# Optimization experiments

Measured on AMD Instinct MI355X. Metric: run time of the kernel, lower is better.

## Reference

```python
import jax, jax.numpy as jnp
import numpy as np

B, S, H, NH = 2, 4096, 768, 12
DH = H // NH  # 64


def setup_inputs() -> dict:
    key = jax.random.key(0)
    ks = jax.random.split(key, 7)
    scale = 0.02
    return {
        "x": jax.random.normal(ks[0], (B, S, H), dtype=jnp.float32),
        "Wq": jax.random.normal(ks[1], (H, H), dtype=jnp.float32) * scale,
        "bq": jax.random.normal(ks[2], (H,), dtype=jnp.float32) * scale,
        "Wk": jax.random.normal(ks[3], (H, H), dtype=jnp.float32) * scale,
        "bk": jax.random.normal(ks[4], (H,), dtype=jnp.float32) * scale,
        "Wv": jax.random.normal(ks[5], (H, H), dtype=jnp.float32) * scale,
        "bv": jax.random.normal(ks[6], (H,), dtype=jnp.float32) * scale,
    }


def _split_heads(t):
    # [B,S,H] -> [B,NH,S,DH]
    return t.reshape(B, S, NH, DH).transpose(0, 2, 1, 3)


def reference(x, Wq, bq, Wk, bk, Wv, bv):
    q = _split_heads(x @ Wq + bq)
    k = _split_heads(x @ Wk + bk)
    v = _split_heads(x @ Wv + bv)
    # raw scores + zero additive mask (mask is all zeros, so it is a no-op)
    scores = jnp.einsum("bhqd,bhkd->bhqk", q, k) / jnp.sqrt(jnp.float32(DH))
    probs = jax.nn.softmax(scores, axis=-1)
    ctx = jnp.einsum("bhqk,bhkd->bhqd", probs, v)
    out = ctx.transpose(0, 2, 1, 3).reshape(B, S, H)
    return jnp.tanh(out)
```

## Files before the change

kernel.cpp:

```cpp
#include <hip/hip_runtime.h>
#include <hip/hip_bf16.h>

#define B_ 2
#define S_ 4096
#define H_ 768
#define NH_ 12
#define DH_ 64
#define M_ (B_ * S_)
#define N3_ (3 * H_)
#define NQK 1536
#define K_ H_
#define LOG2E 1.4426950408889634f

typedef __attribute__((ext_vector_type(8))) short short8;
typedef __attribute__((ext_vector_type(4))) float f32x4;
typedef __attribute__((ext_vector_type(16))) float f32x16;
typedef __attribute__((ext_vector_type(4))) unsigned int uint4v;
typedef __attribute__((ext_vector_type(4))) unsigned short ushort4v;

typedef __attribute__((address_space(3))) unsigned int lds_u32;
typedef const __attribute__((address_space(1))) unsigned int glb_u32;

__device__ __forceinline__ unsigned short f2bf(float f) {
    unsigned int u = __builtin_bit_cast(unsigned int, f);
    u += 0x7FFFu + ((u >> 16) & 1u);
    return (unsigned short)(u >> 16);
}
__device__ __forceinline__ unsigned int cvtpk_bf16(float lo, float hi) {
    unsigned int r;
    asm("v_cvt_pk_bf16_f32 %0, %1, %2" : "=v"(r) : "v"(lo), "v"(hi));
    return r;
}
__device__ __forceinline__ void plswap32(unsigned int &x, unsigned int &y) {
    asm("v_permlane32_swap_b32 %0, %1" : "+v"(x), "+v"(y));
}
__device__ __forceinline__ float exp2_fast(float x) {
    float r;
    asm("v_exp_f32 %0, %1" : "=v"(r) : "v"(x));
    return r;
}

__global__ __launch_bounds__(256) void cast_x_kernel(const float* __restrict__ x,
                                                     unsigned short* __restrict__ xb) {
    int i = blockIdx.x * 256 + threadIdx.x;
    float4 v = reinterpret_cast<const float4*>(x)[i];
    ushort4 o;
    o.x = f2bf(v.x); o.y = f2bf(v.y); o.z = f2bf(v.z); o.w = f2bf(v.w);
    reinterpret_cast<ushort4*>(xb)[i] = o;
}

__global__ __launch_bounds__(256) void cast_w_kernel(const float* __restrict__ Wq,
                                                     const float* __restrict__ Wk,
                                                     const float* __restrict__ Wv,
                                                     unsigned short* __restrict__ wt) {
    int id = blockIdx.x * 256 + threadIdx.x;
    int n = id % H_;
    int kb = (id / H_) % 96;
    int wsel = id / (H_ * 96);
    const float* W = (wsel == 0) ? Wq : (wsel == 1) ? Wk : Wv;
    union { unsigned short s[8]; uint4v v; } u;
#pragma unroll
    for (int j = 0; j < 8; j++) u.s[j] = f2bf(W[(size_t)(kb * 8 + j) * H_ + n]);
    *reinterpret_cast<uint4v*>(wt + (size_t)(wsel * H_ + n) * H_ + kb * 8) = u.v;
}

#define GBM 128
#define GBN 128
#define GBK 64

__global__ __launch_bounds__(256) void qkv_gemm_kernel(const unsigned short* __restrict__ xb,
                                                       const unsigned short* __restrict__ wt,
                                                       const float* __restrict__ bq,
                                                       const float* __restrict__ bk,
                                                       const float* __restrict__ bv,
                                                       unsigned short* __restrict__ qk,
                                                       unsigned short* __restrict__ vT) {
    __shared__ unsigned short Asm[GBM * GBK];
    __shared__ unsigned short Bsm[GBN * GBK];
    const int tid = threadIdx.x;
    const int swz = (blockIdx.x & 7) * 144 + (blockIdx.x >> 3);
    const int bm = swz / 18, bn = swz % 18;
    const int w = tid >> 6, l = tid & 63;
    const int wm = w >> 1, wn = w & 1;
    const int lr = l & 15, lk = l >> 4;

    f32x4 zero = {0.f, 0.f, 0.f, 0.f};
    f32x4 acc[4][4];
#pragma unroll
    for (int i = 0; i < 4; i++)
#pragma unroll
        for (int j = 0; j < 4; j++) acc[i][j] = zero;

    const int sr8 = l >> 3;
    const int scolS = (((l & 7) ^ sr8) * 8);
    const unsigned short* aBase = xb + (size_t)(bm * GBM) * K_;
    const unsigned short* bBase = wt + (size_t)(bn * GBN) * K_;

    for (int k0 = 0; k0 < K_; k0 += GBK) {
        __syncthreads();
#pragma unroll
        for (int i = 0; i < 4; i++) {
            const int j = w * 4 + i;
            __builtin_amdgcn_global_load_lds(
                (glb_u32*)(aBase + (size_t)(j * 8 + sr8) * K_ + k0 + scolS),
                (lds_u32*)(&Asm[j * 8 * GBK]), 16, 0, 0);
        }
#pragma unroll
        for (int i = 0; i < 4; i++) {
            const int j = w * 4 + i;
            __builtin_amdgcn_global_load_lds(
                (glb_u32*)(bBase + (size_t)(j * 8 + sr8) * K_ + k0 + scolS),
                (lds_u32*)(&Bsm[j * 8 * GBK]), 16, 0, 0);
        }
        __syncthreads();

#pragma unroll
        for (int ks = 0; ks < 2; ks++) {
            short8 a[4], b[4];
#pragma unroll
            for (int mi = 0; mi < 4; mi++) {
                const int row = wm * 64 + mi * 16 + lr;
                const int slot = ((ks * 4 + lk) ^ (lr & 7)) * 8;
                a[mi] = *reinterpret_cast<const short8*>(&Asm[row * GBK + slot]);
            }
#pragma unroll
            for (int ni = 0; ni < 4; ni++) {
                const int row = wn * 64 + ni * 16 + lr;
                const int slot = ((ks * 4 + lk) ^ (lr & 7)) * 8;
                b[ni] = *reinterpret_cast<const short8*>(&Bsm[row * GBK + slot]);
            }
#pragma unroll
            for (int mi = 0; mi < 4; mi++)
#pragma unroll
                for (int ni = 0; ni < 4; ni++)
                    acc[mi][ni] = __builtin_amdgcn_mfma_f32_16x16x32_bf16(a[mi], b[ni], acc[mi][ni], 0, 0, 0);
        }
    }

    if (bn < 12) {
#pragma unroll
        for (int ni = 0; ni < 4; ni++) {
            const int col = bn * GBN + wn * 64 + ni * 16 + lr;
            const bool isQ = (col < H_);
            const float bias = isQ ? bq[col] : bk[col - H_];
            const float scl = isQ ? (0.125f * LOG2E) : 1.0f;
#pragma unroll
            for (int mi = 0; mi < 4; mi++) {
#pragma unroll
                for (int i = 0; i < 4; i++) {
                    const int row = bm * GBM + wm * 64 + mi * 16 + lk * 4 + i;
                    qk[(size_t)row * NQK + col] = f2bf((acc[mi][ni][i] + bias) * scl);
                }
            }
        }
    } else {
#pragma unroll
        for (int ni = 0; ni < 4; ni++) {
            const int c = bn * GBN - 2 * H_ + wn * 64 + ni * 16 + lr;
            const int h = c >> 6, d = c & 63;
            const float bias = bv[c];
#pragma unroll
            for (int mi = 0; mi < 4; mi++) {
                const int row0 = bm * GBM + wm * 64 + mi * 16 + lk * 4;
                const int b = row0 >> 12, s0 = row0 & (S_ - 1);
                union { unsigned short s[4]; ushort4v v; } u;
#pragma unroll
                for (int i = 0; i < 4; i++) u.s[i] = f2bf(acc[mi][ni][i] + bias);
                *reinterpret_cast<ushort4v*>(vT + ((size_t)(b * NH_ + h) * DH_ + d) * S_ + s0) = u.v;
            }
        }
    }
}

#define QW 32
#define QB 128
#define KB 64

__global__ __launch_bounds__(256, 2) void attn_kernel(const unsigned short* __restrict__ qk,
                                                      const unsigned short* __restrict__ vT,
                                                      float* __restrict__ out) {
    __shared__ unsigned short Ksm[KB * 64];
    __shared__ unsigned short Vsm[DH_ * KB];
    const int tid = threadIdx.x;
    const int w = tid >> 6, l = tid & 63;
    const int ln = l & 31, hi = l >> 5;
    const int swz = (blockIdx.x & 7) * 96 + (blockIdx.x >> 3);
    const int qt = swz & 31, bh = swz >> 5;
    const int b = bh / NH_, h = bh % NH_;

    const unsigned short* Qg = qk + (size_t)b * S_ * NQK + h * DH_;
    const unsigned short* Kg = Qg + H_;
    const unsigned short* Vg = vT + (size_t)bh * DH_ * S_;

    const int qrow = qt * QB + w * QW + ln;
    short8 qf[4];
    {
        const unsigned short* qp = Qg + (size_t)qrow * NQK + hi * 8;
#pragma unroll
        for (int dk = 0; dk < 4; dk++)
            qf[dk] = *reinterpret_cast<const short8*>(qp + dk * 16);
    }

    const f32x16 fz = {0,0,0,0,0,0,0,0,0,0,0,0,0,0,0,0};
    f32x16 o0 = fz, o1 = fz;
    float m_ = 0.f, lsum = 0.f;

    const int srow = tid >> 2;
    const int sd = (tid & 3) * 16;
    const unsigned short* kgp = Kg + (size_t)srow * NQK + sd;
    const unsigned short* vgp = Vg + (size_t)srow * S_ + sd;
    const int sidx0 = (srow * 64 + sd) ^ ((srow & 7) << 3);
    const int sidx1 = (srow * 64 + sd + 8) ^ ((srow & 7) << 3);

    uint4v kr0 = *reinterpret_cast<const uint4v*>(kgp);
    uint4v kr1 = *reinterpret_cast<const uint4v*>(kgp + 8);
    uint4v vr0 = *reinterpret_cast<const uint4v*>(vgp);
    uint4v vr1 = *reinterpret_cast<const uint4v*>(vgp + 8);

    for (int kt = 0; kt < S_; kt += KB) {
        asm volatile("" ::: "memory");
        __builtin_amdgcn_s_barrier();
        asm volatile("" ::: "memory");
        *reinterpret_cast<uint4v*>(&Ksm[sidx0]) = kr0;
        *reinterpret_cast<uint4v*>(&Ksm[sidx1]) = kr1;
        *reinterpret_cast<uint4v*>(&Vsm[sidx0]) = vr0;
        *reinterpret_cast<uint4v*>(&Vsm[sidx1]) = vr1;
        if (kt + KB < S_) {
            kr0 = *reinterpret_cast<const uint4v*>(kgp + (size_t)(kt + KB) * NQK);
            kr1 = *reinterpret_cast<const uint4v*>(kgp + (size_t)(kt + KB) * NQK + 8);
            vr0 = *reinterpret_cast<const uint4v*>(vgp + kt + KB);
            vr1 = *reinterpret_cast<const uint4v*>(vgp + kt + KB + 8);
        }
        asm volatile("s_waitcnt lgkmcnt(0)" ::: "memory");
        __builtin_amdgcn_s_barrier();
        asm volatile("" ::: "memory");

        f32x16 cm;
#pragma unroll
        for (int r = 0; r < 16; r++) cm[r] = -m_;
        f32x16 s0 = cm, s1 = cm;
#pragma unroll
        for (int dk = 0; dk < 4; dk++) {
            const int col = dk * 16 + hi * 8;
            short8 kf0 = *reinterpret_cast<const short8*>(&Ksm[(ln * 64 + col) ^ ((ln & 7) << 3)]);
            short8 kf1 = *reinterpret_cast<const short8*>(&Ksm[((32 + ln) * 64 + col) ^ ((ln & 7) << 3)]);
            s0 = __builtin_amdgcn_mfma_f32_32x32x16_bf16(kf0, qf[dk], s0, 0, 0, 0);
            s1 = __builtin_amdgcn_mfma_f32_32x32x16_bf16(kf1, qf[dk], s1, 0, 0, 0);
        }

        float pm = -1e30f;
#pragma unroll
        for (int r = 0; r < 16; r += 4)
            pm = fmaxf(fmaxf(pm, s0[r]), fmaxf(fmaxf(s0[r+1], s0[r+2]), s0[r+3]));
#pragma unroll
        for (int r = 0; r < 16; r += 4)
            pm = fmaxf(fmaxf(pm, s1[r]), fmaxf(fmaxf(s1[r+1], s1[r+2]), s1[r+3]));
        pm = fmaxf(pm, __shfl_xor(pm, 32));
        if (!__all(pm <= 8.0f)) {
            const float step = fmaxf(pm, 0.f);
            const float corr = exp2_fast(-step);
            m_ += step;
            lsum *= corr;
#pragma unroll
            for (int r = 0; r < 16; r++) { s0[r] -= step; s1[r] -= step; }
#pragma unroll
            for (int r = 0; r < 16; r++) {
                const float c = __shfl(corr, (r & 3) + 8 * (r >> 2) + 4 * hi);
                o0[r] *= c; o1[r] *= c;
            }
        }
        float p[32];
        float rs = 0.f;
#pragma unroll
        for (int r = 0; r < 16; r++) { p[r] = exp2_fast(s0[r]); rs += p[r]; }
#pragma unroll
        for (int r = 0; r < 16; r++) { p[16 + r] = exp2_fast(s1[r]); rs += p[16 + r]; }
        rs += __shfl_xor(rs, 32);
        lsum += rs;

        short8 pa[4];
#pragma unroll
        for (int half = 0; half < 2; half++) {
            unsigned int c0 = cvtpk_bf16(p[half*16+0],  p[half*16+1]);
            unsigned int c1 = cvtpk_bf16(p[half*16+2],  p[half*16+3]);
            unsigned int c2 = cvtpk_bf16(p[half*16+4],  p[half*16+5]);
            unsigned int c3 = cvtpk_bf16(p[half*16+6],  p[half*16+7]);
            unsigned int c4 = cvtpk_bf16(p[half*16+8],  p[half*16+9]);
            unsigned int c5 = cvtpk_bf16(p[half*16+10], p[half*16+11]);
            unsigned int c6 = cvtpk_bf16(p[half*16+12], p[half*16+13]);
            unsigned int c7 = cvtpk_bf16(p[half*16+14], p[half*16+15]);
            plswap32(c0, c2); plswap32(c1, c3);
            plswap32(c4, c6); plswap32(c5, c7);
            union { unsigned int u[4]; short8 v; } ua, ub;
            ua.u[0] = c0; ua.u[1] = c1; ua.u[2] = c2; ua.u[3] = c3;
            ub.u[0] = c4; ub.u[1] = c5; ub.u[2] = c6; ub.u[3] = c7;
            pa[half * 2]     = ua.v;
            pa[half * 2 + 1] = ub.v;
        }

#pragma unroll
        for (int s4 = 0; s4 < 4; s4++) {
            const int kcol = s4 * 16 + hi * 8;
            short8 vf0 = *reinterpret_cast<const short8*>(&Vsm[(ln * 64 + kcol) ^ ((ln & 7) << 3)]);
            short8 vf1 = *reinterpret_cast<const short8*>(&Vsm[((32 + ln) * 64 + kcol) ^ ((ln & 7) << 3)]);
            o0 = __builtin_amdgcn_mfma_f32_32x32x16_bf16(pa[s4], vf0, o0, 0, 0, 0);
            o1 = __builtin_amdgcn_mfma_f32_32x32x16_bf16(pa[s4], vf1, o1, 0, 0, 0);
        }
    }

    float* op = out + ((size_t)b * S_ + qt * QB + w * QW) * H_ + h * DH_;
#pragma unroll
    for (int r = 0; r < 16; r++) {
        const int q = (r & 3) + 8 * (r >> 2) + 4 * hi;
        const float inv = 1.0f / __shfl(lsum, q);
        op[(size_t)q * H_ + ln]      = tanhf(o0[r] * inv);
        op[(size_t)q * H_ + 32 + ln] = tanhf(o1[r] * inv);
    }
}

extern "C" void kernel_launch(void* const* d_in, const int* in_sizes, int n_in,
                              void* d_out, int out_size, void* d_ws, size_t ws_size,
                              hipStream_t stream) {
    const float* x  = (const float*)d_in[0];
    const float* Wq = (const float*)d_in[1];
    const float* bq = (const float*)d_in[2];
    const float* Wk = (const float*)d_in[3];
    const float* bk = (const float*)d_in[4];
    const float* Wv = (const float*)d_in[5];
    const float* bv = (const float*)d_in[6];
    float* out = (float*)d_out;

    char* ws = (char*)d_ws;
    unsigned short* xb = (unsigned short*)ws;
    size_t off = (size_t)M_ * K_ * 2;
    unsigned short* wt = (unsigned short*)(ws + off);
    off += (size_t)N3_ * K_ * 2;
    unsigned short* qkb = (unsigned short*)(ws + off);
    off += (size_t)M_ * NQK * 2;
    unsigned short* vTb = (unsigned short*)(ws + off);

    cast_x_kernel<<<dim3((M_ * K_) / 4 / 256), dim3(256), 0, stream>>>(x, xb);
    cast_w_kernel<<<dim3((3 * H_ * 96) / 256), dim3(256), 0, stream>>>(Wq, Wk, Wv, wt);
    qkv_gemm_kernel<<<dim3((M_ / GBM) * (N3_ / GBN)), dim3(256), 0, stream>>>(xb, wt, bq, bk, bv, qkb, vTb);
    attn_kernel<<<dim3(B_ * NH_ * (S_ / QB)), dim3(256), 0, stream>>>(qkb, vTb, out);
}
```

Before: 270.8 us.

## Double-buffer LDS tiles in QKV GEMM to overlap loads with MFMA

Adds a second LDS buffer for the A and B tiles in the QKV projection GEMM. The next K tile is prefetched through global_load_lds while MFMAs run on the current tile, and the per-iteration syncthreads pair becomes one waitcnt plus barrier. This targets exposed global-load latency in the GEMM main loop, at the cost of doubling LDS use per block (64KB), which may lower occupancy. The full unroll of the 12-step loop also raises code size.

New measurement: 266.6 us. About the same (-1.6%).

```diff
diff --git a/kernel.cpp b/kernel.cpp
--- a/kernel.cpp
+++ b/kernel.cpp
@@ -67,6 +67,7 @@
 #define GBM 128
 #define GBN 128
 #define GBK 64
+#define NT (K_ / GBK)
 
 __global__ __launch_bounds__(256) void qkv_gemm_kernel(const unsigned short* __restrict__ xb,
                                                        const unsigned short* __restrict__ wt,
@@ -75,8 +76,8 @@
                                                        const float* __restrict__ bv,
                                                        unsigned short* __restrict__ qk,
                                                        unsigned short* __restrict__ vT) {
-    __shared__ unsigned short Asm[GBM * GBK];
-    __shared__ unsigned short Bsm[GBN * GBK];
+    __shared__ unsigned short Asm[2][GBM * GBK];
+    __shared__ unsigned short Bsm[2][GBN * GBK];
     const int tid = threadIdx.x;
     const int swz = (blockIdx.x & 7) * 144 + (blockIdx.x >> 3);
     const int bm = swz / 18, bn = swz % 18;
@@ -92,27 +93,37 @@
         for (int j = 0; j < 4; j++) acc[i][j] = zero;
 
     const int sr8 = l >> 3;
-    const int scolS = (((l & 7) ^ sr8) * 8);
-    const unsigned short* aBase = xb + (size_t)(bm * GBM) * K_;
-    const unsigned short* bBase = wt + (size_t)(bn * GBN) * K_;
-
-    for (int k0 = 0; k0 < K_; k0 += GBK) {
-        __syncthreads();
-#pragma unroll
-        for (int i = 0; i < 4; i++) {
-            const int j = w * 4 + i;
-            __builtin_amdgcn_global_load_lds(
-                (glb_u32*)(aBase + (size_t)(j * 8 + sr8) * K_ + k0 + scolS),
-                (lds_u32*)(&Asm[j * 8 * GBK]), 16, 0, 0);
-        }
-#pragma unroll
-        for (int i = 0; i < 4; i++) {
-            const int j = w * 4 + i;
-            __builtin_amdgcn_global_load_lds(
-                (glb_u32*)(bBase + (size_t)(j * 8 + sr8) * K_ + k0 + scolS),
-                (lds_u32*)(&Bsm[j * 8 * GBK]), 16, 0, 0);
-        }
-        __syncthreads();
+    const int scolS = ((l & 7) ^ sr8) * 8;
+    const unsigned short* aSrc = xb + (size_t)(bm * GBM + sr8) * K_ + scolS;
+    const unsigned short* bSrc = wt + (size_t)(bn * GBN + sr8) * K_ + scolS;
+
+#define STAGE(buf, k0)                                                             \
+    do {                                                                           \
+        _Pragma("unroll")                                                          \
+        for (int i_ = 0; i_ < 4; i_++) {                                           \
+            const int j_ = w * 4 + i_;                                             \
+            __builtin_amdgcn_global_load_lds(                                      \
+                (glb_u32*)(aSrc + (size_t)j_ * 8 * K_ + (k0)),                     \
+                (lds_u32*)(&Asm[buf][j_ * 8 * GBK]), 16, 0, 0);                    \
+        }                                                                          \
+        _Pragma("unroll")                                                          \
+        for (int i_ = 0; i_ < 4; i_++) {                                           \
+            const int j_ = w * 4 + i_;                                             \
+            __builtin_amdgcn_global_load_lds(                                      \
+                (glb_u32*)(bSrc + (size_t)j_ * 8 * K_ + (k0)),                     \
+                (lds_u32*)(&Bsm[buf][j_ * 8 * GBK]), 16, 0, 0);                    \
+        }                                                                          \
+    } while (0)
+
+    STAGE(0, 0);
+    asm volatile("s_waitcnt vmcnt(0)" ::: "memory");
+    __builtin_amdgcn_s_barrier();
+    asm volatile("" ::: "memory");
+
+#pragma unroll
+    for (int t = 0; t < NT; ++t) {
+        const int cur = t & 1;
+        if (t + 1 < NT) STAGE(cur ^ 1, (t + 1) * GBK);
 
 #pragma unroll
         for (int ks = 0; ks < 2; ks++) {
@@ -121,13 +132,13 @@
             for (int mi = 0; mi < 4; mi++) {
                 const int row = wm * 64 + mi * 16 + lr;
                 const int slot = ((ks * 4 + lk) ^ (lr & 7)) * 8;
-                a[mi] = *reinterpret_cast<const short8*>(&Asm[row * GBK + slot]);
+                a[mi] = *reinterpret_cast<const short8*>(&Asm[cur][row * GBK + slot]);
             }
 #pragma unroll
             for (int ni = 0; ni < 4; ni++) {
                 const int row = wn * 64 + ni * 16 + lr;
                 const int slot = ((ks * 4 + lk) ^ (lr & 7)) * 8;
-                b[ni] = *reinterpret_cast<const short8*>(&Bsm[row * GBK + slot]);
+                b[ni] = *reinterpret_cast<const short8*>(&Bsm[cur][row * GBK + slot]);
             }
 #pragma unroll
             for (int mi = 0; mi < 4; mi++)
@@ -135,7 +146,14 @@
                 for (int ni = 0; ni < 4; ni++)
                     acc[mi][ni] = __builtin_amdgcn_mfma_f32_16x16x32_bf16(a[mi], b[ni], acc[mi][ni], 0, 0, 0);
         }
-    }
+
+        if (t + 1 < NT) {
+            asm volatile("s_waitcnt vmcnt(0)" ::: "memory");
+            __builtin_amdgcn_s_barrier();
+            asm volatile("" ::: "memory");
+        }
+    }
+#undef STAGE
 
     if (bn < 12) {
 #pragma unroll
```

## Split attention keys across two wave groups and merge partial softmax results

Applied to the files above, without the earlier changes.

The attention kernel now runs 512 threads per block, and each group of four waves processes half of the key sequence with its own K/V LDS buffers. The two partial outputs are combined at the end through LDS using the online-softmax max and sum rescaling. This is meant to raise parallelism and latency hiding per query tile, at the cost of an extra merge step and more LDS and register pressure. The QKV GEMM is also changed: it uses a smaller K tile with padded LDS rows and plain register-staged loads in place of direct global-to-LDS loads. s_setprio hints are added around the MFMA sections.

New measurement: 441.4 us. +63.0%, slower.

```diff
diff --git a/kernel.cpp b/kernel.cpp
--- a/kernel.cpp
+++ b/kernel.cpp
@@ -18,9 +18,6 @@
 typedef __attribute__((ext_vector_type(4))) unsigned int uint4v;
 typedef __attribute__((ext_vector_type(4))) unsigned short ushort4v;
 
-typedef __attribute__((address_space(3))) unsigned int lds_u32;
-typedef const __attribute__((address_space(1))) unsigned int glb_u32;
-
 __device__ __forceinline__ unsigned short f2bf(float f) {
     unsigned int u = __builtin_bit_cast(unsigned int, f);
     u += 0x7FFFu + ((u >> 16) & 1u);
@@ -66,7 +63,8 @@
 
 #define GBM 128
 #define GBN 128
-#define GBK 64
+#define GBK 32
+#define LDT 40
 
 __global__ __launch_bounds__(256) void qkv_gemm_kernel(const unsigned short* __restrict__ xb,
                                                        const unsigned short* __restrict__ wt,
@@ -75,8 +73,8 @@
                                                        const float* __restrict__ bv,
                                                        unsigned short* __restrict__ qk,
                                                        unsigned short* __restrict__ vT) {
-    __shared__ unsigned short Asm[GBM * GBK];
-    __shared__ unsigned short Bsm[GBN * GBK];
+    __shared__ unsigned short Asm[GBM * LDT];
+    __shared__ unsigned short Bsm[GBN * LDT];
     const int tid = threadIdx.x;
     const int swz = (blockIdx.x & 7) * 144 + (blockIdx.x >> 3);
     const int bm = swz / 18, bn = swz % 18;
@@ -91,50 +89,35 @@
 #pragma unroll
         for (int j = 0; j < 4; j++) acc[i][j] = zero;
 
-    const int sr8 = l >> 3;
-    const int scolS = (((l & 7) ^ sr8) * 8);
-    const unsigned short* aBase = xb + (size_t)(bm * GBM) * K_;
-    const unsigned short* bBase = wt + (size_t)(bn * GBN) * K_;
+    const int srow = tid >> 2;
+    const int scol = (tid & 3) * 8;
+    const unsigned short* aG = xb + (size_t)(bm * GBM + srow) * K_ + scol;
+    const unsigned short* bG = wt + (size_t)(bn * GBN + srow) * K_ + scol;
 
     for (int k0 = 0; k0 < K_; k0 += GBK) {
         __syncthreads();
-#pragma unroll
-        for (int i = 0; i < 4; i++) {
-            const int j = w * 4 + i;
-            __builtin_amdgcn_global_load_lds(
-                (glb_u32*)(aBase + (size_t)(j * 8 + sr8) * K_ + k0 + scolS),
-                (lds_u32*)(&Asm[j * 8 * GBK]), 16, 0, 0);
-        }
-#pragma unroll
-        for (int i = 0; i < 4; i++) {
-            const int j = w * 4 + i;
-            __builtin_amdgcn_global_load_lds(
-                (glb_u32*)(bBase + (size_t)(j * 8 + sr8) * K_ + k0 + scolS),
-                (lds_u32*)(&Bsm[j * 8 * GBK]), 16, 0, 0);
-        }
+        *reinterpret_cast<uint4v*>(&Asm[srow * LDT + scol]) =
+            *reinterpret_cast<const uint4v*>(aG + k0);
+        *reinterpret_cast<uint4v*>(&Asm[(srow + 64) * LDT + scol]) =
+            *reinterpret_cast<const uint4v*>(aG + (size_t)64 * K_ + k0);
+        *reinterpret_cast<uint4v*>(&Bsm[srow * LDT + scol]) =
+            *reinterpret_cast<const uint4v*>(bG + k0);
+        *reinterpret_cast<uint4v*>(&Bsm[(srow + 64) * LDT + scol]) =
+            *reinterpret_cast<const uint4v*>(bG + (size_t)64 * K_ + k0);
         __syncthreads();
 
-#pragma unroll
-        for (int ks = 0; ks < 2; ks++) {
-            short8 a[4], b[4];
-#pragma unroll
-            for (int mi = 0; mi < 4; mi++) {
-                const int row = wm * 64 + mi * 16 + lr;
-                const int slot = ((ks * 4 + lk) ^ (lr & 7)) * 8;
-                a[mi] = *reinterpret_cast<const short8*>(&Asm[row * GBK + slot]);
-            }
-#pragma unroll
-            for (int ni = 0; ni < 4; ni++) {
-                const int row = wn * 64 + ni * 16 + lr;
-                const int slot = ((ks * 4 + lk) ^ (lr & 7)) * 8;
-                b[ni] = *reinterpret_cast<const short8*>(&Bsm[row * GBK + slot]);
-            }
-#pragma unroll
-            for (int mi = 0; mi < 4; mi++)
-#pragma unroll
-                for (int ni = 0; ni < 4; ni++)
-                    acc[mi][ni] = __builtin_amdgcn_mfma_f32_16x16x32_bf16(a[mi], b[ni], acc[mi][ni], 0, 0, 0);
-        }
+        short8 a[4], b[4];
+#pragma unroll
+        for (int mi = 0; mi < 4; mi++)
+            a[mi] = *reinterpret_cast<const short8*>(&Asm[(wm * 64 + mi * 16 + lr) * LDT + lk * 8]);
+#pragma unroll
+        for (int ni = 0; ni < 4; ni++)
+            b[ni] = *reinterpret_cast<const short8*>(&Bsm[(wn * 64 + ni * 16 + lr) * LDT + lk * 8]);
+#pragma unroll
+        for (int mi = 0; mi < 4; mi++)
+#pragma unroll
+            for (int ni = 0; ni < 4; ni++)
+                acc[mi][ni] = __builtin_amdgcn_mfma_f32_16x16x32_bf16(a[mi], b[ni], acc[mi][ni], 0, 0, 0);
     }
 
     if (bn < 12) {
@@ -175,14 +158,18 @@
 #define QW 32
 #define QB 128
 #define KB 64
-
-__global__ __launch_bounds__(256, 2) void attn_kernel(const unsigned short* __restrict__ qk,
+#define HKEYS 2048
+
+__global__ __launch_bounds__(512, 4) void attn_kernel(const unsigned short* __restrict__ qk,
                                                       const unsigned short* __restrict__ vT,
                                                       float* __restrict__ out) {
-    __shared__ unsigned short Ksm[KB * 64];
-    __shared__ unsigned short Vsm[DH_ * KB];
+    __shared__ __align__(16) float MrgF[4 * 34 * 64];
+    char* SB = (char*)MrgF;
     const int tid = threadIdx.x;
-    const int w = tid >> 6, l = tid & 63;
+    const int w = tid >> 6;
+    const int g = w >> 2;
+    const int wb = w & 3;
+    const int l = tid & 63;
     const int ln = l & 31, hi = l >> 5;
     const int swz = (blockIdx.x & 7) * 96 + (blockIdx.x >> 3);
     const int qt = swz & 31, bh = swz >> 5;
@@ -192,7 +179,10 @@
     const unsigned short* Kg = Qg + H_;
     const unsigned short* Vg = vT + (size_t)bh * DH_ * S_;
 
-    const int qrow = qt * QB + w * QW + ln;
+    unsigned short* Ks = (unsigned short*)(SB + g * 16384);
+    unsigned short* Vs = (unsigned short*)(SB + g * 16384 + 8192);
+
+    const int qrow = qt * QB + wb * QW + ln;
     short8 qf[4];
     {
         const unsigned short* qp = Qg + (size_t)qrow * NQK + hi * 8;
@@ -205,10 +195,11 @@
     f32x16 o0 = fz, o1 = fz;
     float m_ = 0.f, lsum = 0.f;
 
-    const int srow = tid >> 2;
-    const int sd = (tid & 3) * 16;
-    const unsigned short* kgp = Kg + (size_t)srow * NQK + sd;
-    const unsigned short* vgp = Vg + (size_t)srow * S_ + sd;
+    const int t8 = tid & 255;
+    const int srow = t8 >> 2;
+    const int sd = (t8 & 3) * 16;
+    const unsigned short* kgp = Kg + (size_t)(g * HKEYS + srow) * NQK + sd;
+    const unsigned short* vgp = Vg + (size_t)srow * S_ + g * HKEYS + sd;
     const int sidx0 = (srow * 64 + sd) ^ ((srow & 7) << 3);
     const int sidx1 = (srow * 64 + sd + 8) ^ ((srow & 7) << 3);
 
@@ -217,15 +208,15 @@
     uint4v vr0 = *reinterpret_cast<const uint4v*>(vgp);
     uint4v vr1 = *reinterpret_cast<const uint4v*>(vgp + 8);
 
-    for (int kt = 0; kt < S_; kt += KB) {
+    for (int kt = 0; kt < HKEYS; kt += KB) {
         asm volatile("" ::: "memory");
         __builtin_amdgcn_s_barrier();
         asm volatile("" ::: "memory");
-        *reinterpret_cast<uint4v*>(&Ksm[sidx0]) = kr0;
-        *reinterpret_cast<uint4v*>(&Ksm[sidx1]) = kr1;
-        *reinterpret_cast<uint4v*>(&Vsm[sidx0]) = vr0;
-        *reinterpret_cast<uint4v*>(&Vsm[sidx1]) = vr1;
-        if (kt + KB < S_) {
+        *reinterpret_cast<uint4v*>(&Ks[sidx0]) = kr0;
+        *reinterpret_cast<uint4v*>(&Ks[sidx1]) = kr1;
+        *reinterpret_cast<uint4v*>(&Vs[sidx0]) = vr0;
+        *reinterpret_cast<uint4v*>(&Vs[sidx1]) = vr1;
+        if (kt + KB < HKEYS) {
             kr0 = *reinterpret_cast<const uint4v*>(kgp + (size_t)(kt + KB) * NQK);
             kr1 = *reinterpret_cast<const uint4v*>(kgp + (size_t)(kt + KB) * NQK + 8);
             vr0 = *reinterpret_cast<const uint4v*>(vgp + kt + KB);
@@ -239,14 +230,16 @@
 #pragma unroll
         for (int r = 0; r < 16; r++) cm[r] = -m_;
         f32x16 s0 = cm, s1 = cm;
+        __builtin_amdgcn_s_setprio(1);
 #pragma unroll
         for (int dk = 0; dk < 4; dk++) {
             const int col = dk * 16 + hi * 8;
-            short8 kf0 = *reinterpret_cast<const short8*>(&Ksm[(ln * 64 + col) ^ ((ln & 7) << 3)]);
-            short8 kf1 = *reinterpret_cast<const short8*>(&Ksm[((32 + ln) * 64 + col) ^ ((ln & 7) << 3)]);
+            short8 kf0 = *reinterpret_cast<const short8*>(&Ks[(ln * 64 + col) ^ ((ln & 7) << 3)]);
+            short8 kf1 = *reinterpret_cast<const short8*>(&Ks[((32 + ln) * 64 + col) ^ ((ln & 7) << 3)]);
             s0 = __builtin_amdgcn_mfma_f32_32x32x16_bf16(kf0, qf[dk], s0, 0, 0, 0);
             s1 = __builtin_amdgcn_mfma_f32_32x32x16_bf16(kf1, qf[dk], s1, 0, 0, 0);
         }
+        __builtin_amdgcn_s_setprio(0);
 
         float pm = -1e30f;
 #pragma unroll
@@ -298,23 +291,48 @@
             pa[half * 2 + 1] = ub.v;
         }
 
+        __builtin_amdgcn_s_setprio(1);
 #pragma unroll
         for (int s4 = 0; s4 < 4; s4++) {
             const int kcol = s4 * 16 + hi * 8;
-            short8 vf0 = *reinterpret_cast<const short8*>(&Vsm[(ln * 64 + kcol) ^ ((ln & 7) << 3)]);
-            short8 vf1 = *reinterpret_cast<const short8*>(&Vsm[((32 + ln) * 64 + kcol) ^ ((ln & 7) << 3)]);
+            short8 vf0 = *reinterpret_cast<const short8*>(&Vs[(ln * 64 + kcol) ^ ((ln & 7) << 3)]);
+            short8 vf1 = *reinterpret_cast<const short8*>(&Vs[((32 + ln) * 64 + kcol) ^ ((ln & 7) << 3)]);
             o0 = __builtin_amdgcn_mfma_f32_32x32x16_bf16(pa[s4], vf0, o0, 0, 0, 0);
             o1 = __builtin_amdgcn_mfma_f32_32x32x16_bf16(pa[s4], vf1, o1, 0, 0, 0);
         }
-    }
-
-    float* op = out + ((size_t)b * S_ + qt * QB + w * QW) * H_ + h * DH_;
-#pragma unroll
-    for (int r = 0; r < 16; r++) {
-        const int q = (r & 3) + 8 * (r >> 2) + 4 * hi;
-        const float inv = 1.0f / __shfl(lsum, q);
-        op[(size_t)q * H_ + ln]      = tanhf(o0[r] * inv);
-        op[(size_t)q * H_ + 32 + ln] = tanhf(o1[r] * inv);
+        __builtin_amdgcn_s_setprio(0);
+    }
+
+    __syncthreads();
+    if (g == 1) {
+#pragma unroll
+        for (int r = 0; r < 16; r++) {
+            MrgF[(wb * 34 + r) * 64 + l]      = o0[r];
+            MrgF[(wb * 34 + 16 + r) * 64 + l] = o1[r];
+        }
+        MrgF[(wb * 34 + 32) * 64 + l] = m_;
+        MrgF[(wb * 34 + 33) * 64 + l] = lsum;
+    }
+    __syncthreads();
+    if (g == 0) {
+        const float mB = MrgF[(wb * 34 + 32) * 64 + l];
+        const float lB = MrgF[(wb * 34 + 33) * 64 + l];
+        const float mM = fmaxf(m_, mB);
+        const float cA = exp2_fast(m_ - mM);
+        const float cB = exp2_fast(mB - mM);
+        const float lM = lsum * cA + lB * cB;
+        float* op = out + ((size_t)b * S_ + qt * QB + wb * QW) * H_ + h * DH_;
+#pragma unroll
+        for (int r = 0; r < 16; r++) {
+            const int q = (r & 3) + 8 * (r >> 2) + 4 * hi;
+            const float fA = __shfl(cA, q);
+            const float fB = __shfl(cB, q);
+            const float inv = 1.0f / __shfl(lM, q);
+            const float vb0 = MrgF[(wb * 34 + r) * 64 + l];
+            const float vb1 = MrgF[(wb * 34 + 16 + r) * 64 + l];
+            op[(size_t)q * H_ + ln]      = tanhf((o0[r] * fA + vb0 * fB) * inv);
+            op[(size_t)q * H_ + 32 + ln] = tanhf((o1[r] * fA + vb1 * fB) * inv);
+        }
     }
 }
 
@@ -342,5 +360,5 @@
     cast_x_kernel<<<dim3((M_ * K_) / 4 / 256), dim3(256), 0, stream>>>(x, xb);
     cast_w_kernel<<<dim3((3 * H_ * 96) / 256), dim3(256), 0, stream>>>(Wq, Wk, Wv, wt);
     qkv_gemm_kernel<<<dim3((M_ / GBM) * (N3_ / GBN)), dim3(256), 0, stream>>>(xb, wt, bq, bk, bv, qkb, vTb);
-    attn_kernel<<<dim3(B_ * NH_ * (S_ / QB)), dim3(256), 0, stream>>>(qkb, vTb, out);
-}
+    attn_kernel<<<dim3(B_ * NH_ * (S_ / QB)), dim3(512), 0, stream>>>(qkb, vTb, out);
+}
```
